# Performance work log

Measured on AMD Instinct MI355X. Metric: run time of the kernel, lower is better.

Reference implementation:

```python
import jax, jax.numpy as jnp
import numpy as np

EPS = 1e-5
GROUPS = 8


def setup_inputs() -> dict:
    key = jax.random.key(0)
    ks = jax.random.split(key, 3)
    b, c, h, w = 8, 256, 64, 64
    x = jax.random.normal(ks[0], (b, c, h, w), dtype=jnp.float32)
    # 1x1 convs are just channel matmuls; store weights as [out_ch, in_ch]
    qkv_w = jax.random.normal(ks[1], (3 * c, c), dtype=jnp.float32) * (c ** -0.5)
    qkv_b = jnp.zeros((3 * c,), dtype=jnp.float32)
    out_w = jax.random.normal(ks[2], (c, c), dtype=jnp.float32) * (c ** -0.5)
    out_b = jnp.zeros((c,), dtype=jnp.float32)
    gn_w = jnp.ones((c,), dtype=jnp.float32)
    gn_b = jnp.zeros((c,), dtype=jnp.float32)
    return {"x": x, "gn_w": gn_w, "gn_b": gn_b, "qkv_w": qkv_w,
            "qkv_b": qkv_b, "out_w": out_w, "out_b": out_b}


def _group_norm(x, gn_w, gn_b):
    # x: [b, c, h, w]; normalize per (group, sample) over (c//g, h, w)
    b, c, h, w = x.shape
    xg = x.reshape(b, GROUPS, c // GROUPS, h * w)
    mean = xg.mean(axis=(2, 3), keepdims=True)
    var = xg.var(axis=(2, 3), keepdims=True)
    xn = (xg - mean) * jax.lax.rsqrt(var + EPS)
    xn = xn.reshape(b, c, h * w)
    return xn * gn_w[None, :, None] + gn_b[None, :, None]


def reference(x, gn_w, gn_b, qkv_w, qkv_b, out_w, out_b):
    b, c, h, w = x.shape
    scale = 1.0 / np.sqrt(c).astype(np.float32)  # matches channels ** -0.5
    nx = _group_norm(x, gn_w, gn_b)                       # [b, c, n]
    qkv = jnp.einsum('oc,bcn->bon', qkv_w, nx) + qkv_b[None, :, None]
    q, k, v = qkv[:, :c], qkv[:, c:2 * c], qkv[:, 2 * c:]  # each [b, c, n]
    attn = jnp.einsum('bci,bcj->bij', q, k) * scale        # [b, n, n]
    attn = jax.nn.softmax(attn, axis=-1)
    out = jnp.einsum('bij,bcj->bci', attn, v)              # [b, c, n]
    out = jnp.einsum('oc,bcn->bon', out_w, out) + out_b[None, :, None]
    return out.reshape(b, c, h, w) + x
```

## Files before the change

### kernel.cpp

```cpp
#include <hip/hip_runtime.h>
#include <math.h>


#define Bn 8
#define Cn 256
#define HWn 4096
#define Gn 8
#define CPGn 32
#define Mqkv 768
#define EPSf 1e-5f
#define QSCALEf 0.0625f
#define RTHR 8.0f

typedef short bf16x8 __attribute__((ext_vector_type(8)));
typedef float f32x4 __attribute__((ext_vector_type(4)));
typedef float f32x16 __attribute__((ext_vector_type(16)));

__device__ __forceinline__ unsigned short f2bf(float f) {
  union { float f; unsigned u; } v; v.f = f;
  unsigned r = v.u + 0x7FFFu + ((v.u >> 16) & 1u);
  return (unsigned short)(r >> 16);
}

__device__ __forceinline__ int cvt_pk_bf16(float lo, float hi) {
  int d;
  asm("v_cvt_pk_bf16_f32 %0, %1, %2" : "=v"(d) : "v"(lo), "v"(hi));
  return d;
}

__global__ __launch_bounds__(1024)
void gn_stats_kernel(const float* __restrict__ x, const float* __restrict__ gn_w,
                     const float* __restrict__ gn_b, float* __restrict__ s_out,
                     float* __restrict__ t_out) {
  const int b = blockIdx.x / Gn, g = blockIdx.x % Gn;
  const float4* base = (const float4*)(x + ((size_t)(b * Cn + g * CPGn)) * HWn);
  const int n4 = CPGn * HWn / 4;
  float sum = 0.f, sq = 0.f;
  for (int i = threadIdx.x; i < n4; i += 1024) {
    float4 v = base[i];
    sum += (v.x + v.y) + (v.z + v.w);
    sq  += (v.x * v.x + v.y * v.y) + (v.z * v.z + v.w * v.w);
  }
  __shared__ float ss[1024], s2[1024];
  ss[threadIdx.x] = sum; s2[threadIdx.x] = sq;
  __syncthreads();
  for (int off = 512; off > 0; off >>= 1) {
    if ((int)threadIdx.x < off) {
      ss[threadIdx.x] += ss[threadIdx.x + off];
      s2[threadIdx.x] += s2[threadIdx.x + off];
    }
    __syncthreads();
  }
  if (threadIdx.x < CPGn) {
    const float inv_n = 1.f / (float)(CPGn * HWn);
    float mean = ss[0] * inv_n;
    float var  = s2[0] * inv_n - mean * mean;
    float rstd = rsqrtf(var + EPSf);
    int c = g * CPGn + (int)threadIdx.x;
    float sc = gn_w[c] * rstd;
    s_out[b * Cn + c] = sc;
    t_out[b * Cn + c] = gn_b[c] - mean * sc;
  }
}

__global__ __launch_bounds__(256)
void affine_transpose_kernel(const float* __restrict__ x, const float* __restrict__ s_aff,
                             const float* __restrict__ t_aff, unsigned short* __restrict__ nxT) {
  const int bid = blockIdx.x;
  const int b = bid & 7, r = bid >> 3;
  const int c0 = (r & 3) * 64, n0 = (r >> 2) * 64;
  const int tid = threadIdx.x;
  __shared__ unsigned int ld32[64][33];
  const float* xb = x + ((size_t)(b * Cn + c0)) * HWn + n0;
  const int cl0 = tid >> 4, nn = (tid & 15) * 4;
#pragma unroll
  for (int it = 0; it < 4; ++it) {
    int cl = cl0 + 16 * it;
    int c = c0 + cl;
    float sc = s_aff[b * Cn + c], sh = t_aff[b * Cn + c];
    float4 v = *(const float4*)(xb + (size_t)cl * HWn + nn);
    ld32[cl][(nn >> 1) + 0] = (unsigned)cvt_pk_bf16(v.x * sc + sh, v.y * sc + sh);
    ld32[cl][(nn >> 1) + 1] = (unsigned)cvt_pk_bf16(v.z * sc + sh, v.w * sc + sh);
  }
  __syncthreads();
#pragma unroll
  for (int it = 0; it < 2; ++it) {
    int chunk = tid + 256 * it;
    int n = chunk >> 3, cg = chunk & 7;
    union { unsigned short u[8]; bf16x8 v; } o;
#pragma unroll
    for (int k = 0; k < 8; ++k) {
      unsigned w32 = ld32[cg * 8 + k][n >> 1];
      o.u[k] = (unsigned short)((n & 1) ? (w32 >> 16) : (w32 & 0xffffu));
    }
    *(bf16x8*)(nxT + ((size_t)(b * HWn + n0 + n)) * Cn + c0 + cg * 8) = o.v;
  }
}

__global__ __launch_bounds__(256, 2)
void qkv_gemm_kernel(const unsigned short* __restrict__ nxT, const float* __restrict__ w,
                     const float* __restrict__ wb, unsigned short* __restrict__ Qt,
                     unsigned short* __restrict__ Kt, unsigned short* __restrict__ Vb) {
  const int bid = blockIdx.x;
  const int b = bid & 7, r = bid >> 3;
  const int n0 = (r & 63) * 64, m0 = (r >> 6) * 128;
  const int tid = threadIdx.x;
  const int wv = tid >> 6, l = tid & 63;
  const int l15 = l & 15, lq = l >> 4;
  const int ob = m0 + wv * 32;

  bf16x8 wf[2][8];
#pragma unroll
  for (int g = 0; g < 2; ++g) {
    const float* wr = w + (size_t)(ob + g * 16 + l15) * Cn + lq * 8;
#pragma unroll
    for (int kc = 0; kc < 8; ++kc) {
      float4 a = *(const float4*)(wr + kc * 32);
      float4 c4 = *(const float4*)(wr + kc * 32 + 4);
      union { int w4[4]; bf16x8 v; } u;
      u.w4[0] = cvt_pk_bf16(a.x, a.y);  u.w4[1] = cvt_pk_bf16(a.z, a.w);
      u.w4[2] = cvt_pk_bf16(c4.x, c4.y); u.w4[3] = cvt_pk_bf16(c4.z, c4.w);
      wf[g][kc] = u.v;
    }
  }

  const unsigned short* nb = nxT + (size_t)b * HWn * Cn + lq * 8;
  f32x4 acc[2][4];
#pragma unroll
  for (int g = 0; g < 2; ++g)
#pragma unroll
    for (int s = 0; s < 4; ++s) acc[g][s] = (f32x4)(0.f);

  const bool isV = (m0 >= 512);
#pragma unroll
  for (int s = 0; s < 4; ++s) {
    const unsigned short* np = nb + (size_t)(n0 + s * 16 + l15) * Cn;
#pragma unroll
    for (int kc = 0; kc < 8; ++kc) {
      bf16x8 xf = *(const bf16x8*)(np + kc * 32);
      if (!isV) {
        acc[0][s] = __builtin_amdgcn_mfma_f32_16x16x32_bf16(wf[0][kc], xf, acc[0][s], 0, 0, 0);
        acc[1][s] = __builtin_amdgcn_mfma_f32_16x16x32_bf16(wf[1][kc], xf, acc[1][s], 0, 0, 0);
      } else {
        acc[0][s] = __builtin_amdgcn_mfma_f32_16x16x32_bf16(xf, wf[0][kc], acc[0][s], 0, 0, 0);
        acc[1][s] = __builtin_amdgcn_mfma_f32_16x16x32_bf16(xf, wf[1][kc], acc[1][s], 0, 0, 0);
      }
    }
  }

  if (!isV) {
    unsigned short* dst = (m0 < 256) ? Qt : Kt;
    const float scl = (m0 < 256) ? QSCALEf : 1.0f;
#pragma unroll
    for (int g = 0; g < 2; ++g) {
      int cb = ((ob + g * 16) & 255) + lq * 4;
      float b0 = wb[ob + g * 16 + lq * 4 + 0];
      float b1 = wb[ob + g * 16 + lq * 4 + 1];
      float b2 = wb[ob + g * 16 + lq * 4 + 2];
      float b3 = wb[ob + g * 16 + lq * 4 + 3];
#pragma unroll
      for (int s = 0; s < 4; ++s) {
        int n = n0 + s * 16 + l15;
        ushort4 pk;
        pk.x = f2bf((acc[g][s][0] + b0) * scl);
        pk.y = f2bf((acc[g][s][1] + b1) * scl);
        pk.z = f2bf((acc[g][s][2] + b2) * scl);
        pk.w = f2bf((acc[g][s][3] + b3) * scl);
        *(ushort4*)(dst + ((size_t)(b * HWn + n)) * Cn + cb) = pk;
      }
    }
  } else {
#pragma unroll
    for (int g = 0; g < 2; ++g) {
      int o = ob + g * 16 + l15;
      int c = o - 512;
      float bias = wb[o];
#pragma unroll
      for (int s = 0; s < 4; ++s) {
        int n = n0 + s * 16 + lq * 4;
        ushort4 pk;
        pk.x = f2bf(acc[g][s][0] + bias);
        pk.y = f2bf(acc[g][s][1] + bias);
        pk.z = f2bf(acc[g][s][2] + bias);
        pk.w = f2bf(acc[g][s][3] + bias);
        *(ushort4*)(Vb + ((size_t)(b * Cn + c)) * HWn + n) = pk;
      }
    }
  }
}

__global__ __launch_bounds__(256, 2)
void attn_kernel(const unsigned short* __restrict__ Qt,
                 const unsigned short* __restrict__ Kt,
                 const unsigned short* __restrict__ Vb,
                 unsigned short* __restrict__ outp) {
  const int bid = blockIdx.x;
  const int b = bid & 7, i0 = (bid >> 3) * 64;
  const int tid = threadIdx.x;
  const int wv = tid >> 6, l = tid & 63;
  const int l31 = l & 31, hi = l >> 5;
  const int rg = wv >> 1, cw = wv & 1;

  __shared__ unsigned short Ks[8192];
  __shared__ unsigned short Vs[8192];
  char* KsB = (char*)Ks;
  char* VsB = (char*)Vs;

  const unsigned short* Qb = Qt + ((size_t)b * HWn + i0) * Cn;
  const unsigned short* Kb = Kt + (size_t)b * HWn * Cn;
  const unsigned short* Vg = Vb + (size_t)b * Cn * HWn;

  bf16x8 qf[16];
  {
    const unsigned short* qrow = Qb + (size_t)(rg * 32 + l31) * Cn + hi * 8;
#pragma unroll
    for (int kc = 0; kc < 16; ++kc) qf[kc] = *(const bf16x8*)(qrow + kc * 16);
  }

  const unsigned short* gK = Kb + (size_t)(tid & 31) * Cn + (tid >> 5) * 8;
  const unsigned short* gV = Vg + (size_t)((tid >> 7) * 32 + (tid & 31)) * HWn
                                + ((tid >> 5) & 3) * 8;

  bf16x8 kst[4], vst[4];
#pragma unroll
  for (int q = 0; q < 4; ++q) kst[q] = *(const bf16x8*)(gK + q * 64);
#pragma unroll
  for (int q = 0; q < 4; ++q) vst[q] = *(const bf16x8*)(gV + (size_t)q * 64 * HWn);
  gK += 32 * Cn; gV += 32;

  f32x16 o0 = (f32x16)(0.f), o1 = (f32x16)(0.f);
  f32x16 o2 = (f32x16)(0.f), o3 = (f32x16)(0.f);
  float m_i = -INFINITY, l_i = 0.f;
  const int vbase = cw * 4 * 2048;

#pragma unroll 1
  for (int t = 0; t < 128; ++t) {
#pragma unroll
    for (int q = 0; q < 4; ++q) *(bf16x8*)(KsB + tid * 16 + q * 4096) = kst[q];
#pragma unroll
    for (int q = 0; q < 4; ++q) *(bf16x8*)(VsB + tid * 16 + q * 4096) = vst[q];
    __syncthreads();
    if (t < 127) {
#pragma unroll
      for (int q = 0; q < 4; ++q) kst[q] = *(const bf16x8*)(gK + q * 64);
#pragma unroll
      for (int q = 0; q < 4; ++q) vst[q] = *(const bf16x8*)(gV + (size_t)q * 64 * HWn);
      gK += 32 * Cn; gV += 32;
    }

    f32x16 sa = (f32x16)(0.f);
#pragma unroll
    for (int kc = 0; kc < 16; ++kc) {
      bf16x8 kf = *(const bf16x8*)(KsB + l * 16 + kc * 1024);
      sa = __builtin_amdgcn_mfma_f32_32x32x16_bf16(kf, qf[kc], sa, 0, 0, 0);
    }

    float p[16];
#pragma unroll
    for (int r = 0; r < 16; ++r) p[r] = sa[r];
    float rm = p[0];
#pragma unroll
    for (int r = 1; r < 16; ++r) rm = fmaxf(rm, p[r]);
    rm = fmaxf(rm, __shfl_xor(rm, 32));
    if (!__all(rm - m_i <= RTHR)) {
      float mn = fmaxf(m_i, rm);
      float alpha = __expf(m_i - mn);
      m_i = mn;
      l_i *= alpha;
#pragma unroll
      for (int r = 0; r < 16; ++r) {
        o0[r] *= alpha; o1[r] *= alpha; o2[r] *= alpha; o3[r] *= alpha;
      }
    }
    float rs = 0.f;
#pragma unroll
    for (int r = 0; r < 16; ++r) { p[r] = __expf(p[r] - m_i); rs += p[r]; }
    rs += __shfl_xor(rs, 32);
    l_i += rs;

    int d0 = cvt_pk_bf16(p[0],  p[1]),  d1 = cvt_pk_bf16(p[2],  p[3]);
    int d2 = cvt_pk_bf16(p[4],  p[5]),  d3 = cvt_pk_bf16(p[6],  p[7]);
    int d4 = cvt_pk_bf16(p[8],  p[9]),  d5 = cvt_pk_bf16(p[10], p[11]);
    int d6 = cvt_pk_bf16(p[12], p[13]), d7 = cvt_pk_bf16(p[14], p[15]);
    int x0 = __shfl_xor(d0, 32), x1 = __shfl_xor(d1, 32);
    int x2 = __shfl_xor(d2, 32), x3 = __shfl_xor(d3, 32);
    int x4 = __shfl_xor(d4, 32), x5 = __shfl_xor(d5, 32);
    int x6 = __shfl_xor(d6, 32), x7 = __shfl_xor(d7, 32);
    union { int w[4]; bf16x8 v; } pf0, pf1;
    pf0.w[0] = hi ? x2 : d0; pf0.w[1] = hi ? x3 : d1;
    pf0.w[2] = hi ? d2 : x0; pf0.w[3] = hi ? d3 : x1;
    pf1.w[0] = hi ? x6 : d4; pf1.w[1] = hi ? x7 : d5;
    pf1.w[2] = hi ? d6 : x4; pf1.w[3] = hi ? d7 : x5;

    {
      bf16x8 vf0 = *(const bf16x8*)(VsB + l * 16 + vbase + 0 * 2048);
      bf16x8 vf1 = *(const bf16x8*)(VsB + l * 16 + vbase + 0 * 2048 + 1024);
      o0 = __builtin_amdgcn_mfma_f32_32x32x16_bf16(vf0, pf0.v, o0, 0, 0, 0);
      o0 = __builtin_amdgcn_mfma_f32_32x32x16_bf16(vf1, pf1.v, o0, 0, 0, 0);
      vf0 = *(const bf16x8*)(VsB + l * 16 + vbase + 1 * 2048);
      vf1 = *(const bf16x8*)(VsB + l * 16 + vbase + 1 * 2048 + 1024);
      o1 = __builtin_amdgcn_mfma_f32_32x32x16_bf16(vf0, pf0.v, o1, 0, 0, 0);
      o1 = __builtin_amdgcn_mfma_f32_32x32x16_bf16(vf1, pf1.v, o1, 0, 0, 0);
      vf0 = *(const bf16x8*)(VsB + l * 16 + vbase + 2 * 2048);
      vf1 = *(const bf16x8*)(VsB + l * 16 + vbase + 2 * 2048 + 1024);
      o2 = __builtin_amdgcn_mfma_f32_32x32x16_bf16(vf0, pf0.v, o2, 0, 0, 0);
      o2 = __builtin_amdgcn_mfma_f32_32x32x16_bf16(vf1, pf1.v, o2, 0, 0, 0);
      vf0 = *(const bf16x8*)(VsB + l * 16 + vbase + 3 * 2048);
      vf1 = *(const bf16x8*)(VsB + l * 16 + vbase + 3 * 2048 + 1024);
      o3 = __builtin_amdgcn_mfma_f32_32x32x16_bf16(vf0, pf0.v, o3, 0, 0, 0);
      o3 = __builtin_amdgcn_mfma_f32_32x32x16_bf16(vf1, pf1.v, o3, 0, 0, 0);
    }
    __syncthreads();
  }

  float il = 1.f / l_i;
  unsigned short* ob = outp + ((size_t)b * HWn + (size_t)(i0 + rg * 32 + l31)) * Cn;
  const int cb0 = cw * 128 + 4 * hi;
#pragma unroll
  for (int rq = 0; rq < 4; ++rq) {
    ushort4 s0v, s1v, s2v, s3v;
    s0v.x = f2bf(o0[rq * 4 + 0] * il); s0v.y = f2bf(o0[rq * 4 + 1] * il);
    s0v.z = f2bf(o0[rq * 4 + 2] * il); s0v.w = f2bf(o0[rq * 4 + 3] * il);
    s1v.x = f2bf(o1[rq * 4 + 0] * il); s1v.y = f2bf(o1[rq * 4 + 1] * il);
    s1v.z = f2bf(o1[rq * 4 + 2] * il); s1v.w = f2bf(o1[rq * 4 + 3] * il);
    s2v.x = f2bf(o2[rq * 4 + 0] * il); s2v.y = f2bf(o2[rq * 4 + 1] * il);
    s2v.z = f2bf(o2[rq * 4 + 2] * il); s2v.w = f2bf(o2[rq * 4 + 3] * il);
    s3v.x = f2bf(o3[rq * 4 + 0] * il); s3v.y = f2bf(o3[rq * 4 + 1] * il);
    s3v.z = f2bf(o3[rq * 4 + 2] * il); s3v.w = f2bf(o3[rq * 4 + 3] * il);
    *(ushort4*)(ob + cb0 + 0 * 32 + 8 * rq) = s0v;
    *(ushort4*)(ob + cb0 + 1 * 32 + 8 * rq) = s1v;
    *(ushort4*)(ob + cb0 + 2 * 32 + 8 * rq) = s2v;
    *(ushort4*)(ob + cb0 + 3 * 32 + 8 * rq) = s3v;
  }
}

__global__ __launch_bounds__(256, 2)
void out_gemm_kernel(const unsigned short* __restrict__ tmpT, const float* __restrict__ w,
                     const float* __restrict__ wb, const float* __restrict__ xres,
                     float* __restrict__ y) {
  const int bid = blockIdx.x;
  const int b = bid & 7, r = bid >> 3;
  const int n0 = (r & 63) * 64, m0 = (r >> 6) * 128;
  const int tid = threadIdx.x;
  const int wv = tid >> 6, l = tid & 63;
  const int l15 = l & 15, lq = l >> 4;
  const int ob = m0 + wv * 32;

  bf16x8 wf[2][8];
#pragma unroll
  for (int g = 0; g < 2; ++g) {
    const float* wr = w + (size_t)(ob + g * 16 + l15) * Cn + lq * 8;
#pragma unroll
    for (int kc = 0; kc < 8; ++kc) {
      float4 a = *(const float4*)(wr + kc * 32);
      float4 c4 = *(const float4*)(wr + kc * 32 + 4);
      union { int w4[4]; bf16x8 v; } u;
      u.w4[0] = cvt_pk_bf16(a.x, a.y);  u.w4[1] = cvt_pk_bf16(a.z, a.w);
      u.w4[2] = cvt_pk_bf16(c4.x, c4.y); u.w4[3] = cvt_pk_bf16(c4.z, c4.w);
      wf[g][kc] = u.v;
    }
  }

  const unsigned short* tb = tmpT + (size_t)b * HWn * Cn + lq * 8;
  f32x4 acc[2][4];
#pragma unroll
  for (int g = 0; g < 2; ++g)
#pragma unroll
    for (int s = 0; s < 4; ++s) acc[g][s] = (f32x4)(0.f);

#pragma unroll
  for (int s = 0; s < 4; ++s) {
    const unsigned short* tp = tb + (size_t)(n0 + s * 16 + l15) * Cn;
#pragma unroll
    for (int kc = 0; kc < 8; ++kc) {
      bf16x8 tf = *(const bf16x8*)(tp + kc * 32);
      acc[0][s] = __builtin_amdgcn_mfma_f32_16x16x32_bf16(tf, wf[0][kc], acc[0][s], 0, 0, 0);
      acc[1][s] = __builtin_amdgcn_mfma_f32_16x16x32_bf16(tf, wf[1][kc], acc[1][s], 0, 0, 0);
    }
  }

#pragma unroll
  for (int g = 0; g < 2; ++g) {
    int o = ob + g * 16 + l15;
    float bias = wb[o];
#pragma unroll
    for (int s = 0; s < 4; ++s) {
      int n = n0 + s * 16 + lq * 4;
      size_t idx = ((size_t)(b * Cn + o)) * HWn + n;
      float4 xr = *(const float4*)(xres + idx);
      float4 out;
      out.x = acc[g][s][0] + bias + xr.x;
      out.y = acc[g][s][1] + bias + xr.y;
      out.z = acc[g][s][2] + bias + xr.z;
      out.w = acc[g][s][3] + bias + xr.w;
      *(float4*)(y + idx) = out;
    }
  }
}

extern "C" void kernel_launch(void* const* d_in, const int* in_sizes, int n_in,
                              void* d_out, int out_size, void* d_ws, size_t ws_size,
                              hipStream_t stream) {
  (void)in_sizes; (void)n_in; (void)out_size; (void)ws_size;
  const float* x     = (const float*)d_in[0];
  const float* gn_w  = (const float*)d_in[1];
  const float* gn_b  = (const float*)d_in[2];
  const float* qkv_w = (const float*)d_in[3];
  const float* qkv_b = (const float*)d_in[4];
  const float* out_w = (const float*)d_in[5];
  const float* out_b = (const float*)d_in[6];
  float* out = (float*)d_out;

  char* ws = (char*)d_ws;
  float* s_aff = (float*)ws;
  float* t_aff = s_aff + Bn * Cn;
  unsigned short* Qt  = (unsigned short*)(ws + 16384);
  unsigned short* Kt  = Qt  + (size_t)Bn * HWn * Cn;
  unsigned short* Vb  = Kt  + (size_t)Bn * HWn * Cn;
  unsigned short* nxT = Vb  + (size_t)Bn * HWn * Cn;
  unsigned short* tmpT = nxT + (size_t)Bn * HWn * Cn;

  gn_stats_kernel<<<dim3(Bn * Gn), 1024, 0, stream>>>(x, gn_w, gn_b, s_aff, t_aff);
  affine_transpose_kernel<<<dim3(2048), 256, 0, stream>>>(x, s_aff, t_aff, nxT);
  qkv_gemm_kernel<<<dim3(3072), 256, 0, stream>>>(nxT, qkv_w, qkv_b, Qt, Kt, Vb);
  attn_kernel<<<dim3(512), 256, 0, stream>>>(Qt, Kt, Vb, tmpT);
  out_gemm_kernel<<<dim3(1024), 256, 0, stream>>>(tmpT, out_w, out_b, x, out);
}
```

Before: 420.1 us.

## Double-buffer K/V shared tiles and split QK accumulation chain

Shared K/V tiles are double-buffered: the next tile is written into the alternate buffer midway through the iteration, which removes one of the two barriers per iteration and hides the LDS store behind compute. The QK^T MFMA chain is split into two independent accumulators to cut dependent-MFMA latency. s_setprio raises wave priority around the MFMA blocks. LDS use doubles to 64KB per block, which may limit occupancy against the 2-blocks launch bound.

```diff
diff --git a/kernel.cpp b/kernel.cpp
--- a/kernel.cpp
+++ b/kernel.cpp
@@ -201,8 +201,8 @@
   const int l31 = l & 31, hi = l >> 5;
   const int rg = wv >> 1, cw = wv & 1;
 
-  __shared__ unsigned short Ks[8192];
-  __shared__ unsigned short Vs[8192];
+  __shared__ unsigned short Ks[16384];
+  __shared__ unsigned short Vs[16384];
   char* KsB = (char*)Ks;
   char* VsB = (char*)Vs;
 
@@ -228,18 +228,21 @@
   for (int q = 0; q < 4; ++q) vst[q] = *(const bf16x8*)(gV + (size_t)q * 64 * HWn);
   gK += 32 * Cn; gV += 32;
 
+#pragma unroll
+  for (int q = 0; q < 4; ++q) *(bf16x8*)(KsB + tid * 16 + q * 4096) = kst[q];
+#pragma unroll
+  for (int q = 0; q < 4; ++q) *(bf16x8*)(VsB + tid * 16 + q * 4096) = vst[q];
+  __syncthreads();
+
   f32x16 o0 = (f32x16)(0.f), o1 = (f32x16)(0.f);
   f32x16 o2 = (f32x16)(0.f), o3 = (f32x16)(0.f);
   float m_i = -INFINITY, l_i = 0.f;
-  const int vbase = cw * 4 * 2048;
+  const int vhalf = cw * 8192;
 
 #pragma unroll 1
   for (int t = 0; t < 128; ++t) {
-#pragma unroll
-    for (int q = 0; q < 4; ++q) *(bf16x8*)(KsB + tid * 16 + q * 4096) = kst[q];
-#pragma unroll
-    for (int q = 0; q < 4; ++q) *(bf16x8*)(VsB + tid * 16 + q * 4096) = vst[q];
-    __syncthreads();
+    const int cb = (t & 1) * 16384;
+    const int nb = 16384 - cb;
     if (t < 127) {
 #pragma unroll
       for (int q = 0; q < 4; ++q) kst[q] = *(const bf16x8*)(gK + q * 64);
@@ -248,16 +251,20 @@
       gK += 32 * Cn; gV += 32;
     }
 
-    f32x16 sa = (f32x16)(0.f);
-#pragma unroll
-    for (int kc = 0; kc < 16; ++kc) {
-      bf16x8 kf = *(const bf16x8*)(KsB + l * 16 + kc * 1024);
-      sa = __builtin_amdgcn_mfma_f32_32x32x16_bf16(kf, qf[kc], sa, 0, 0, 0);
-    }
+    f32x16 sa0 = (f32x16)(0.f), sa1 = (f32x16)(0.f);
+    __builtin_amdgcn_s_setprio(1);
+#pragma unroll
+    for (int kc = 0; kc < 8; ++kc) {
+      bf16x8 kf0 = *(const bf16x8*)(KsB + cb + l * 16 + kc * 1024);
+      bf16x8 kf1 = *(const bf16x8*)(KsB + cb + l * 16 + (kc + 8) * 1024);
+      sa0 = __builtin_amdgcn_mfma_f32_32x32x16_bf16(kf0, qf[kc], sa0, 0, 0, 0);
+      sa1 = __builtin_amdgcn_mfma_f32_32x32x16_bf16(kf1, qf[kc + 8], sa1, 0, 0, 0);
+    }
+    __builtin_amdgcn_s_setprio(0);
 
     float p[16];
 #pragma unroll
-    for (int r = 0; r < 16; ++r) p[r] = sa[r];
+    for (int r = 0; r < 16; ++r) p[r] = sa0[r] + sa1[r];
     float rm = p[0];
 #pragma unroll
     for (int r = 1; r < 16; ++r) rm = fmaxf(rm, p[r]);
@@ -277,6 +284,13 @@
     for (int r = 0; r < 16; ++r) { p[r] = __expf(p[r] - m_i); rs += p[r]; }
     rs += __shfl_xor(rs, 32);
     l_i += rs;
+
+    if (t < 127) {
+#pragma unroll
+      for (int q = 0; q < 4; ++q) *(bf16x8*)(KsB + nb + tid * 16 + q * 4096) = kst[q];
+#pragma unroll
+      for (int q = 0; q < 4; ++q) *(bf16x8*)(VsB + nb + tid * 16 + q * 4096) = vst[q];
+    }
 
     int d0 = cvt_pk_bf16(p[0],  p[1]),  d1 = cvt_pk_bf16(p[2],  p[3]);
     int d2 = cvt_pk_bf16(p[4],  p[5]),  d3 = cvt_pk_bf16(p[6],  p[7]);
@@ -292,24 +306,27 @@
     pf1.w[0] = hi ? x6 : d4; pf1.w[1] = hi ? x7 : d5;
     pf1.w[2] = hi ? d6 : x4; pf1.w[3] = hi ? d7 : x5;
 
+    __builtin_amdgcn_s_setprio(1);
     {
-      bf16x8 vf0 = *(const bf16x8*)(VsB + l * 16 + vbase + 0 * 2048);
-      bf16x8 vf1 = *(const bf16x8*)(VsB + l * 16 + vbase + 0 * 2048 + 1024);
+      const char* vb = VsB + cb + vhalf + l * 16;
+      bf16x8 vf0 = *(const bf16x8*)(vb + 0 * 2048);
+      bf16x8 vf1 = *(const bf16x8*)(vb + 0 * 2048 + 1024);
       o0 = __builtin_amdgcn_mfma_f32_32x32x16_bf16(vf0, pf0.v, o0, 0, 0, 0);
       o0 = __builtin_amdgcn_mfma_f32_32x32x16_bf16(vf1, pf1.v, o0, 0, 0, 0);
-      vf0 = *(const bf16x8*)(VsB + l * 16 + vbase + 1 * 2048);
-      vf1 = *(const bf16x8*)(VsB + l * 16 + vbase + 1 * 2048 + 1024);
+      vf0 = *(const bf16x8*)(vb + 1 * 2048);
+      vf1 = *(const bf16x8*)(vb + 1 * 2048 + 1024);
       o1 = __builtin_amdgcn_mfma_f32_32x32x16_bf16(vf0, pf0.v, o1, 0, 0, 0);
       o1 = __builtin_amdgcn_mfma_f32_32x32x16_bf16(vf1, pf1.v, o1, 0, 0, 0);
-      vf0 = *(const bf16x8*)(VsB + l * 16 + vbase + 2 * 2048);
-      vf1 = *(const bf16x8*)(VsB + l * 16 + vbase + 2 * 2048 + 1024);
+      vf0 = *(const bf16x8*)(vb + 2 * 2048);
+      vf1 = *(const bf16x8*)(vb + 2 * 2048 + 1024);
       o2 = __builtin_amdgcn_mfma_f32_32x32x16_bf16(vf0, pf0.v, o2, 0, 0, 0);
       o2 = __builtin_amdgcn_mfma_f32_32x32x16_bf16(vf1, pf1.v, o2, 0, 0, 0);
-      vf0 = *(const bf16x8*)(VsB + l * 16 + vbase + 3 * 2048);
-      vf1 = *(const bf16x8*)(VsB + l * 16 + vbase + 3 * 2048 + 1024);
+      vf0 = *(const bf16x8*)(vb + 3 * 2048);
+      vf1 = *(const bf16x8*)(vb + 3 * 2048 + 1024);
       o3 = __builtin_amdgcn_mfma_f32_32x32x16_bf16(vf0, pf0.v, o3, 0, 0, 0);
       o3 = __builtin_amdgcn_mfma_f32_32x32x16_bf16(vf1, pf1.v, o3, 0, 0, 0);
     }
+    __builtin_amdgcn_s_setprio(0);
     __syncthreads();
   }
 
```

Result: no change. 427.8 us (+1.8%).

## Give attention blocks 128 query rows with each wave owning all channels

Applied to the files above, without the earlier changes.

The attention kernel now handles 128 query rows per block instead of 64. Each of the four waves owns 32 rows and accumulates all 256 output channels in eight MFMA accumulators, instead of pairs of waves splitting the channels. Each K/V tile staged in shared memory is therefore reused by twice as many queries, halving K/V global traffic and removing the duplicated QK^T work across channel-split waves. In exchange, register pressure roughly doubles (launch bounds drop to 1 block/SM) and the grid shrinks to 256 blocks, which may underfill the 256 CUs and reduce latency hiding.

```diff
diff --git a/kernel.cpp b/kernel.cpp
--- a/kernel.cpp
+++ b/kernel.cpp
@@ -189,17 +189,16 @@
   }
 }
 
-__global__ __launch_bounds__(256, 2)
+__global__ __launch_bounds__(256, 1)
 void attn_kernel(const unsigned short* __restrict__ Qt,
                  const unsigned short* __restrict__ Kt,
                  const unsigned short* __restrict__ Vb,
                  unsigned short* __restrict__ outp) {
   const int bid = blockIdx.x;
-  const int b = bid & 7, i0 = (bid >> 3) * 64;
+  const int b = bid & 7, i0 = (bid >> 3) * 128;
   const int tid = threadIdx.x;
   const int wv = tid >> 6, l = tid & 63;
   const int l31 = l & 31, hi = l >> 5;
-  const int rg = wv >> 1, cw = wv & 1;
 
   __shared__ unsigned short Ks[8192];
   __shared__ unsigned short Vs[8192];
@@ -212,14 +211,16 @@
 
   bf16x8 qf[16];
   {
-    const unsigned short* qrow = Qb + (size_t)(rg * 32 + l31) * Cn + hi * 8;
+    const unsigned short* qrow = Qb + (size_t)(wv * 32 + l31) * Cn + hi * 8;
 #pragma unroll
     for (int kc = 0; kc < 16; ++kc) qf[kc] = *(const bf16x8*)(qrow + kc * 16);
   }
 
-  const unsigned short* gK = Kb + (size_t)(tid & 31) * Cn + (tid >> 5) * 8;
-  const unsigned short* gV = Vg + (size_t)((tid >> 7) * 32 + (tid & 31)) * HWn
-                                + ((tid >> 5) & 3) * 8;
+  const int kco = (((tid >> 6) << 1) | ((tid >> 5) & 1));
+  const unsigned short* gK = Kb + (size_t)(tid & 31) * Cn + kco * 8;
+  const int vc  = ((tid >> 7) << 5) | (tid & 31);
+  const int vjo = ((tid >> 5) & 1) | (((tid >> 6) & 1) << 1);
+  const unsigned short* gV = Vg + (size_t)vc * HWn + vjo * 8;
 
   bf16x8 kst[4], vst[4];
 #pragma unroll
@@ -228,10 +229,10 @@
   for (int q = 0; q < 4; ++q) vst[q] = *(const bf16x8*)(gV + (size_t)q * 64 * HWn);
   gK += 32 * Cn; gV += 32;
 
-  f32x16 o0 = (f32x16)(0.f), o1 = (f32x16)(0.f);
-  f32x16 o2 = (f32x16)(0.f), o3 = (f32x16)(0.f);
+  f32x16 oa[8];
+#pragma unroll
+  for (int cb = 0; cb < 8; ++cb) oa[cb] = (f32x16)(0.f);
   float m_i = -INFINITY, l_i = 0.f;
-  const int vbase = cw * 4 * 2048;
 
 #pragma unroll 1
   for (int t = 0; t < 128; ++t) {
@@ -268,9 +269,9 @@
       m_i = mn;
       l_i *= alpha;
 #pragma unroll
-      for (int r = 0; r < 16; ++r) {
-        o0[r] *= alpha; o1[r] *= alpha; o2[r] *= alpha; o3[r] *= alpha;
-      }
+      for (int cb = 0; cb < 8; ++cb)
+#pragma unroll
+        for (int r = 0; r < 16; ++r) oa[cb][r] *= alpha;
     }
     float rs = 0.f;
 #pragma unroll
@@ -292,45 +293,29 @@
     pf1.w[0] = hi ? x6 : d4; pf1.w[1] = hi ? x7 : d5;
     pf1.w[2] = hi ? d6 : x4; pf1.w[3] = hi ? d7 : x5;
 
-    {
-      bf16x8 vf0 = *(const bf16x8*)(VsB + l * 16 + vbase + 0 * 2048);
-      bf16x8 vf1 = *(const bf16x8*)(VsB + l * 16 + vbase + 0 * 2048 + 1024);
-      o0 = __builtin_amdgcn_mfma_f32_32x32x16_bf16(vf0, pf0.v, o0, 0, 0, 0);
-      o0 = __builtin_amdgcn_mfma_f32_32x32x16_bf16(vf1, pf1.v, o0, 0, 0, 0);
-      vf0 = *(const bf16x8*)(VsB + l * 16 + vbase + 1 * 2048);
-      vf1 = *(const bf16x8*)(VsB + l * 16 + vbase + 1 * 2048 + 1024);
-      o1 = __builtin_amdgcn_mfma_f32_32x32x16_bf16(vf0, pf0.v, o1, 0, 0, 0);
-      o1 = __builtin_amdgcn_mfma_f32_32x32x16_bf16(vf1, pf1.v, o1, 0, 0, 0);
-      vf0 = *(const bf16x8*)(VsB + l * 16 + vbase + 2 * 2048);
-      vf1 = *(const bf16x8*)(VsB + l * 16 + vbase + 2 * 2048 + 1024);
-      o2 = __builtin_amdgcn_mfma_f32_32x32x16_bf16(vf0, pf0.v, o2, 0, 0, 0);
-      o2 = __builtin_amdgcn_mfma_f32_32x32x16_bf16(vf1, pf1.v, o2, 0, 0, 0);
-      vf0 = *(const bf16x8*)(VsB + l * 16 + vbase + 3 * 2048);
-      vf1 = *(const bf16x8*)(VsB + l * 16 + vbase + 3 * 2048 + 1024);
-      o3 = __builtin_amdgcn_mfma_f32_32x32x16_bf16(vf0, pf0.v, o3, 0, 0, 0);
-      o3 = __builtin_amdgcn_mfma_f32_32x32x16_bf16(vf1, pf1.v, o3, 0, 0, 0);
+#pragma unroll
+    for (int cb = 0; cb < 8; ++cb) {
+      bf16x8 vf0 = *(const bf16x8*)(VsB + l * 16 + (2 * cb + 0) * 1024);
+      bf16x8 vf1 = *(const bf16x8*)(VsB + l * 16 + (2 * cb + 1) * 1024);
+      oa[cb] = __builtin_amdgcn_mfma_f32_32x32x16_bf16(vf0, pf0.v, oa[cb], 0, 0, 0);
+      oa[cb] = __builtin_amdgcn_mfma_f32_32x32x16_bf16(vf1, pf1.v, oa[cb], 0, 0, 0);
     }
     __syncthreads();
   }
 
   float il = 1.f / l_i;
-  unsigned short* ob = outp + ((size_t)b * HWn + (size_t)(i0 + rg * 32 + l31)) * Cn;
-  const int cb0 = cw * 128 + 4 * hi;
-#pragma unroll
-  for (int rq = 0; rq < 4; ++rq) {
-    ushort4 s0v, s1v, s2v, s3v;
-    s0v.x = f2bf(o0[rq * 4 + 0] * il); s0v.y = f2bf(o0[rq * 4 + 1] * il);
-    s0v.z = f2bf(o0[rq * 4 + 2] * il); s0v.w = f2bf(o0[rq * 4 + 3] * il);
-    s1v.x = f2bf(o1[rq * 4 + 0] * il); s1v.y = f2bf(o1[rq * 4 + 1] * il);
-    s1v.z = f2bf(o1[rq * 4 + 2] * il); s1v.w = f2bf(o1[rq * 4 + 3] * il);
-    s2v.x = f2bf(o2[rq * 4 + 0] * il); s2v.y = f2bf(o2[rq * 4 + 1] * il);
-    s2v.z = f2bf(o2[rq * 4 + 2] * il); s2v.w = f2bf(o2[rq * 4 + 3] * il);
-    s3v.x = f2bf(o3[rq * 4 + 0] * il); s3v.y = f2bf(o3[rq * 4 + 1] * il);
-    s3v.z = f2bf(o3[rq * 4 + 2] * il); s3v.w = f2bf(o3[rq * 4 + 3] * il);
-    *(ushort4*)(ob + cb0 + 0 * 32 + 8 * rq) = s0v;
-    *(ushort4*)(ob + cb0 + 1 * 32 + 8 * rq) = s1v;
-    *(ushort4*)(ob + cb0 + 2 * 32 + 8 * rq) = s2v;
-    *(ushort4*)(ob + cb0 + 3 * 32 + 8 * rq) = s3v;
+  unsigned short* ob = outp + ((size_t)b * HWn + (size_t)(i0 + wv * 32 + l31)) * Cn;
+#pragma unroll
+  for (int cb = 0; cb < 8; ++cb) {
+#pragma unroll
+    for (int g = 0; g < 4; ++g) {
+      ushort4 s4;
+      s4.x = f2bf(oa[cb][g * 4 + 0] * il);
+      s4.y = f2bf(oa[cb][g * 4 + 1] * il);
+      s4.z = f2bf(oa[cb][g * 4 + 2] * il);
+      s4.w = f2bf(oa[cb][g * 4 + 3] * il);
+      *(ushort4*)(ob + cb * 32 + 4 * hi + 8 * g) = s4;
+    }
   }
 }
 
@@ -423,6 +408,6 @@
   gn_stats_kernel<<<dim3(Bn * Gn), 1024, 0, stream>>>(x, gn_w, gn_b, s_aff, t_aff);
   affine_transpose_kernel<<<dim3(2048), 256, 0, stream>>>(x, s_aff, t_aff, nxT);
   qkv_gemm_kernel<<<dim3(3072), 256, 0, stream>>>(nxT, qkv_w, qkv_b, Qt, Kt, Vb);
-  attn_kernel<<<dim3(512), 256, 0, stream>>>(Qt, Kt, Vb, tmpT);
+  attn_kernel<<<dim3(256), 256, 0, stream>>>(Qt, Kt, Vb, tmpT);
   out_gemm_kernel<<<dim3(1024), 256, 0, stream>>>(tmpT, out_w, out_b, x, out);
 }
```

After: 394.1 us, median of 2. 6.2% less time.
